# Kernel tuning notes

Hardware: AMD Instinct MI355X
Metric: run time of the kernel (lower is better)

Reference implementation:

```python
import jax, jax.numpy as jnp
import numpy as np

DIM = 1024
D_INNER = 2048

def setup_inputs() -> dict:
    key = jax.random.key(0)
    ks = jax.random.split(key, 8)
    B, T = 8, 1024
    x = jax.random.normal(ks[0], (B, T, DIM), dtype=jnp.float32)
    h0 = jnp.zeros((B, D_INNER), dtype=jnp.float32)
    # params (xavier-ish scales)
    in_proj_w = jax.random.normal(ks[1], (D_INNER, DIM), dtype=jnp.float32) * (2.0 / (DIM + D_INNER)) ** 0.5
    out_proj_w = jax.random.normal(ks[2], (DIM, D_INNER), dtype=jnp.float32) * (2.0 / (DIM + D_INNER)) ** 0.5
    c_h = jax.random.uniform(ks[3], (D_INNER,), jnp.float32, -0.1, 0.1)
    # spectral normalization as in _init_weights
    c_h = c_h * jnp.minimum(1.0, 0.99 / jnp.abs(jnp.fft.fft(c_h)).max())
    c_x = jax.random.uniform(ks[4], (D_INNER,), jnp.float32, -0.1, 0.1)
    c_x = c_x * jnp.minimum(1.0, 0.99 / jnp.abs(jnp.fft.fft(c_x)).max())
    b = jnp.zeros((D_INNER,), dtype=jnp.float32)
    W_gate = jax.random.normal(ks[5], (D_INNER, D_INNER), dtype=jnp.float32) * (1.0 / D_INNER) ** 0.5
    b_gate = jnp.zeros((D_INNER,), dtype=jnp.float32)
    return {"x": x, "h0": h0, "in_proj_w": in_proj_w, "out_proj_w": out_proj_w,
            "c_h": c_h, "c_x": c_x, "b": b, "W_gate": W_gate, "b_gate": b_gate}

def _circ_apply_fft(fft_c, v):
    # circ(c) @ v along last axis via real FFT; v: [..., D]
    D = v.shape[-1]
    return jnp.fft.irfft(fft_c * jnp.fft.rfft(v, axis=-1), n=D, axis=-1)

def reference(x, h0, in_proj_w, out_proj_w, c_h, c_x, b, W_gate, b_gate):
    B, T, _ = x.shape
    D = h0.shape[-1]
    x_proj = jnp.einsum('btd,ed->bte', x, in_proj_w)  # [B,T,D_inner]
    # gate path (fully parallel over T)
    gate = jax.nn.silu(jnp.einsum('bte,fe->btf', x_proj, W_gate) + b_gate)
    # input circulant contribution, parallel over all tokens
    pre = _circ_apply_fft(jnp.fft.rfft(c_x), x_proj) + b  # [B,T,D]
    fft_ch = jnp.fft.rfft(c_h)

    def step(h_prev, pre_t):
        h_new = jnp.tanh(_circ_apply_fft(fft_ch, h_prev) + pre_t)
        return h_new, h_new

    pre_tbd = jnp.transpose(pre, (1, 0, 2))  # [T,B,D]
    h_final, h_seq = jax.lax.scan(step, h0, pre_tbd)  # h_seq: [T,B,D]
    cell_out = jnp.transpose(h_seq, (1, 0, 2)) * gate  # [B,T,D]
    output = jnp.einsum('bte,de->btd', cell_out, out_proj_w)  # [B,T,dim]
    return output, h_final
```

## Files before the change

kernel.cpp:

```cpp
#include <hip/hip_runtime.h>
#include <cstdint>
#include <cstddef>

#define DI 2048
#define DM 1024
#define BB 8
#define TT 1024
#define ROWS (BB*TT)

typedef short  short8 __attribute__((ext_vector_type(8)));
typedef float  f32x4  __attribute__((ext_vector_type(4)));
typedef float  f32x16 __attribute__((ext_vector_type(16)));

__device__ __forceinline__ unsigned short f2bf(float f) {
  unsigned int u = __builtin_bit_cast(unsigned int, f);
  u = u + 0x7fffu + ((u >> 16) & 1u);
  return (unsigned short)(u >> 16);
}
__device__ __forceinline__ float fast_tanh(float x) {
  float ax = fabsf(x);
  float e  = __expf(-2.0f * ax);
  float t  = (1.0f - e) / (1.0f + e);
  return x < 0.0f ? -t : t;
}
__device__ __forceinline__ float silu_f(float z) {
  return z / (1.0f + __expf(-z));
}
__device__ __forceinline__ unsigned mulpk(unsigned a, unsigned b) {
  float a0 = __builtin_bit_cast(float, a << 16);
  float a1 = __builtin_bit_cast(float, a & 0xffff0000u);
  float b0 = __builtin_bit_cast(float, b << 16);
  float b1 = __builtin_bit_cast(float, b & 0xffff0000u);
  unsigned r0 = f2bf(a0 * b0), r1 = f2bf(a1 * b1);
  return r0 | (r1 << 16);
}
__device__ __forceinline__ uint4 pack8(const unsigned short* q) {
  uint4 p;
  p.x = (unsigned)q[0] | ((unsigned)q[1] << 16);
  p.y = (unsigned)q[2] | ((unsigned)q[3] << 16);
  p.z = (unsigned)q[4] | ((unsigned)q[5] << 16);
  p.w = (unsigned)q[6] | ((unsigned)q[7] << 16);
  return p;
}

__global__ void cast_k(const float* __restrict__ s, short* __restrict__ d, int n4) {
  int i = blockIdx.x * 256 + threadIdx.x;
  if (i >= n4) return;
  float4 f = ((const float4*)s)[i];
  unsigned lo = (unsigned)f2bf(f.x) | ((unsigned)f2bf(f.y) << 16);
  unsigned hi = (unsigned)f2bf(f.z) | ((unsigned)f2bf(f.w) << 16);
  uint2 o; o.x = lo; o.y = hi;
  ((uint2*)d)[i] = o;
}

__global__ void build_cx_k(const float* __restrict__ cx, short* __restrict__ C) {
  int tid = blockIdx.x * 256 + threadIdx.x;
  int n   = tid >> 8;
  int k0  = (tid & 255) * 8;
  unsigned short q[8];
#pragma unroll
  for (int j = 0; j < 8; ++j) q[j] = f2bf(cx[(n - (k0 + j)) & (DI - 1)]);
  *(uint4*)(C + (size_t)n * DI + k0) = pack8(q);
}

__global__ __launch_bounds__(256) void gemm_k(
    const short* __restrict__ A, const short* __restrict__ A2,
    const short* __restrict__ Bt,
    int M, int N, int K, int mode, const float* __restrict__ bias,
    float* __restrict__ outF, short* __restrict__ outH)
{
  __shared__ __align__(16) short As[128 * 40];
  __shared__ __align__(16) short Bs[128 * 40];
  const int tid  = threadIdx.x;
  const int m0   = blockIdx.y * 128, n0 = blockIdx.x * 128;
  const int wave = tid >> 6, lane = tid & 63;
  const int wy = wave >> 1, wx = wave & 1;
  const int l = lane & 15, G = lane >> 4;
  const int srow = tid >> 1, sseg = tid & 1;

  f32x4 acc[4][4];
#pragma unroll
  for (int i = 0; i < 4; ++i)
#pragma unroll
    for (int j = 0; j < 4; ++j) acc[i][j] = (f32x4){0.f, 0.f, 0.f, 0.f};

  for (int k0 = 0; k0 < K; k0 += 32) {
    if (k0) __syncthreads();
    const short* ga = A  + (size_t)(m0 + srow) * K + k0 + sseg * 16;
    const short* gb = Bt + (size_t)(n0 + srow) * K + k0 + sseg * 16;
    uint4 a0 = *(const uint4*)ga;
    uint4 a1 = *(const uint4*)(ga + 8);
    if (A2) {
      const short* g2 = A2 + (size_t)(m0 + srow) * K + k0 + sseg * 16;
      uint4 m0v = *(const uint4*)g2;
      uint4 m1v = *(const uint4*)(g2 + 8);
      a0.x = mulpk(a0.x, m0v.x); a0.y = mulpk(a0.y, m0v.y);
      a0.z = mulpk(a0.z, m0v.z); a0.w = mulpk(a0.w, m0v.w);
      a1.x = mulpk(a1.x, m1v.x); a1.y = mulpk(a1.y, m1v.y);
      a1.z = mulpk(a1.z, m1v.z); a1.w = mulpk(a1.w, m1v.w);
    }
    uint4 b0 = *(const uint4*)gb;
    uint4 b1 = *(const uint4*)(gb + 8);
    *(uint4*)&As[srow * 40 + sseg * 16]     = a0;
    *(uint4*)&As[srow * 40 + sseg * 16 + 8] = a1;
    *(uint4*)&Bs[srow * 40 + sseg * 16]     = b0;
    *(uint4*)&Bs[srow * 40 + sseg * 16 + 8] = b1;
    __syncthreads();
    short8 af[4], bfv[4];
#pragma unroll
    for (int i = 0; i < 4; ++i) af[i]  = *(const short8*)&As[(64 * wy + 16 * i + l) * 40 + 8 * G];
#pragma unroll
    for (int j = 0; j < 4; ++j) bfv[j] = *(const short8*)&Bs[(64 * wx + 16 * j + l) * 40 + 8 * G];
#pragma unroll
    for (int i = 0; i < 4; ++i)
#pragma unroll
      for (int j = 0; j < 4; ++j)
        acc[i][j] = __builtin_amdgcn_mfma_f32_16x16x32_bf16(af[i], bfv[j], acc[i][j], 0, 0, 0);
  }

#pragma unroll
  for (int j = 0; j < 4; ++j) {
    const int c = n0 + 64 * wx + 16 * j + l;
    float bv = 0.f;
    if (mode == 1 || mode == 2) bv = bias[c];
#pragma unroll
    for (int i = 0; i < 4; ++i) {
      const int r0 = m0 + 64 * wy + 16 * i + 4 * G;
#pragma unroll
      for (int v = 0; v < 4; ++v) {
        float z = acc[i][j][v] + bv;
        size_t off = (size_t)(r0 + v) * N + c;
        if (mode == 0)      outH[off] = (short)f2bf(z);
        else if (mode == 2) outH[off] = (short)f2bf(silu_f(z));
        else                outF[off] = z;
      }
    }
  }
}

__global__ __launch_bounds__(512, 2) void fused_k(
    const float* __restrict__ pre, const float* __restrict__ h0,
    const float* __restrict__ ch, short* __restrict__ hseq,
    float* __restrict__ hfin,
    const short* __restrict__ xproj, const short* __restrict__ wg,
    const float* __restrict__ bg, short* __restrict__ gate)
{
  __shared__ __align__(16) char smem[53248];
  const int bid = blockIdx.x;
  const int tid = threadIdx.x;

  if (bid < BB) {
    short* h_lds   = (short*)smem;
    float* pre_lds = (float*)(smem + 4096);
    float* part    = (float*)(smem + 20480);
    const int b = bid;
    const int wid = tid >> 6, lane = tid & 63;
    const int nh = wid & 1, kg = wid >> 1;
    const int L = lane & 31, G2 = lane >> 5;
    const int q = 32 * nh + L;
    const float* preB = pre + (size_t)b * TT * DI;

    short8 av[32];
#pragma unroll
    for (int i = 0; i < 32; ++i) {
      const int kbase = 16 * (32 * kg + i) + 8 * G2;
      short8 v;
#pragma unroll
      for (int j = 0; j < 8; ++j)
        v[j] = (short)f2bf(ch[(L - kbase - j) & (DI - 1)]);
      av[i] = v;
    }

    {
      const int n0 = 4 * tid;
      float4 hv = *(const float4*)(h0 + b * DI + n0);
      unsigned lo = (unsigned)f2bf(hv.x) | ((unsigned)f2bf(hv.y) << 16);
      unsigned hi = (unsigned)f2bf(hv.z) | ((unsigned)f2bf(hv.w) << 16);
      const int blk = tid >> 1;
      const int pblk = blk ^ ((blk >> 3) & 7);
      uint2 w; w.x = lo; w.y = hi;
      *(uint2*)&h_lds[pblk * 8 + 4 * (tid & 1)] = w;
      *(float4*)&pre_lds[n0] = *(const float4*)(preB + n0);
    }
    __syncthreads();

    const int cbase = (G2 + 4 * q + 64 * kg) & 255;

    for (int t = 0; t < TT; ++t) {
      const int cur = t & 1;
      const float* pn = preB + (size_t)(t + 1 < TT ? t + 1 : t) * DI;
      float4 pf = *(const float4*)(pn + 4 * tid);

      f32x16 acc0, acc1;
#pragma unroll
      for (int v = 0; v < 16; ++v) { acc0[v] = 0.f; acc1[v] = 0.f; }
#pragma unroll
      for (int i = 0; i < 32; i += 2) {
        int blkA = (cbase + 2 * i) & 255;
        int blkB = (cbase + 2 * i + 2) & 255;
        int pA = blkA ^ ((blkA >> 3) & 7);
        int pB = blkB ^ ((blkB >> 3) & 7);
        short8 bvA = *(const short8*)&h_lds[pA * 8];
        short8 bvB = *(const short8*)&h_lds[pB * 8];
        acc0 = __builtin_amdgcn_mfma_f32_32x32x16_bf16(av[i],     bvA, acc0, 0, 0, 0);
        acc1 = __builtin_amdgcn_mfma_f32_32x32x16_bf16(av[i + 1], bvB, acc1, 0, 0, 0);
      }
      {
        float* pk = part + kg * DI;
#pragma unroll
        for (int s = 0; s < 4; ++s) {
          const int blk4 = 2 * s + G2 + 8 * q;
          const int p4 = blk4 ^ ((blk4 >> 3) & 7);
          float4 w;
          w.x = acc0[4 * s + 0] + acc1[4 * s + 0];
          w.y = acc0[4 * s + 1] + acc1[4 * s + 1];
          w.z = acc0[4 * s + 2] + acc1[4 * s + 2];
          w.w = acc0[4 * s + 3] + acc1[4 * s + 3];
          *(float4*)&pk[4 * p4] = w;
        }
        *(float4*)&pre_lds[(cur ^ 1) * DI + 4 * tid] = pf;
      }
      __syncthreads();
      {
        const int pb = tid ^ ((tid >> 3) & 7);
        float4 c0 = *(const float4*)&part[4 * pb];
        float4 c1 = *(const float4*)&part[DI + 4 * pb];
        float4 c2 = *(const float4*)&part[2 * DI + 4 * pb];
        float4 c3 = *(const float4*)&part[3 * DI + 4 * pb];
        float4 pr = *(const float4*)&pre_lds[cur * DI + 4 * tid];
        float z0 = c0.x + c1.x + c2.x + c3.x + pr.x;
        float z1 = c0.y + c1.y + c2.y + c3.y + pr.y;
        float z2 = c0.z + c1.z + c2.z + c3.z + pr.z;
        float z3 = c0.w + c1.w + c2.w + c3.w + pr.w;
        float t0 = fast_tanh(z0), t1 = fast_tanh(z1);
        float t2 = fast_tanh(z2), t3 = fast_tanh(z3);
        unsigned lo = (unsigned)f2bf(t0) | ((unsigned)f2bf(t1) << 16);
        unsigned hi = (unsigned)f2bf(t2) | ((unsigned)f2bf(t3) << 16);
        const int blk = tid >> 1;
        const int pblk = blk ^ ((blk >> 3) & 7);
        uint2 w; w.x = lo; w.y = hi;
        *(uint2*)&h_lds[pblk * 8 + 4 * (tid & 1)] = w;
        *(uint2*)(hseq + (size_t)(b * TT + t) * DI + 4 * tid) = w;
        if (t == TT - 1) {
          float4 hf; hf.x = t0; hf.y = t1; hf.z = t2; hf.w = t3;
          *(float4*)(hfin + b * DI + 4 * tid) = hf;
        }
      }
      __syncthreads();
    }
  } else {
    short* As = (short*)smem;
    short* Bs = (short*)(smem + 20480);
    const int wid = tid >> 6, lane = tid & 63;
    const int wy = wid >> 1, wx = wid & 1;
    const int l = lane & 15, G = lane >> 4;

    for (int tile = bid - BB; tile < 512; tile += 248) {
      const int m0 = (tile & 31) * 256, n0 = (tile >> 5) * 128;
      f32x4 acc[4][4];
#pragma unroll
      for (int i = 0; i < 4; ++i)
#pragma unroll
        for (int j = 0; j < 4; ++j) acc[i][j] = (f32x4){0.f, 0.f, 0.f, 0.f};

      for (int k0 = 0; k0 < DI; k0 += 32) {
        __syncthreads();
        const short* ga = xproj + (size_t)(m0 + (tid >> 1)) * DI + k0 + (tid & 1) * 16;
        const short* gb = wg    + (size_t)(n0 + (tid >> 2)) * DI + k0 + (tid & 3) * 8;
        uint4 a0 = *(const uint4*)ga;
        uint4 a1 = *(const uint4*)(ga + 8);
        uint4 b0 = *(const uint4*)gb;
        *(uint4*)&As[(tid >> 1) * 40 + (tid & 1) * 16]     = a0;
        *(uint4*)&As[(tid >> 1) * 40 + (tid & 1) * 16 + 8] = a1;
        *(uint4*)&Bs[(tid >> 2) * 40 + (tid & 3) * 8]      = b0;
        __syncthreads();
        short8 af[4], bfv[4];
#pragma unroll
        for (int i = 0; i < 4; ++i) af[i]  = *(const short8*)&As[(64 * wy + 16 * i + l) * 40 + 8 * G];
#pragma unroll
        for (int j = 0; j < 4; ++j) bfv[j] = *(const short8*)&Bs[(64 * wx + 16 * j + l) * 40 + 8 * G];
#pragma unroll
        for (int i = 0; i < 4; ++i)
#pragma unroll
          for (int j = 0; j < 4; ++j)
            acc[i][j] = __builtin_amdgcn_mfma_f32_16x16x32_bf16(af[i], bfv[j], acc[i][j], 0, 0, 0);
      }
#pragma unroll
      for (int j = 0; j < 4; ++j) {
        const int c = n0 + 64 * wx + 16 * j + l;
        const float bv = bg[c];
#pragma unroll
        for (int i = 0; i < 4; ++i) {
          const int r0 = m0 + 64 * wy + 16 * i + 4 * G;
#pragma unroll
          for (int v = 0; v < 4; ++v) {
            float z = acc[i][j][v] + bv;
            gate[(size_t)(r0 + v) * DI + c] = (short)f2bf(silu_f(z));
          }
        }
      }
      __syncthreads();
    }
  }
}

extern "C" void kernel_launch(void* const* d_in, const int* in_sizes, int n_in,
                              void* d_out, int out_size, void* d_ws, size_t ws_size,
                              hipStream_t stream) {
  const float* x    = (const float*)d_in[0];
  const float* h0   = (const float*)d_in[1];
  const float* win  = (const float*)d_in[2];
  const float* wout = (const float*)d_in[3];
  const float* ch   = (const float*)d_in[4];
  const float* cx   = (const float*)d_in[5];
  const float* bb   = (const float*)d_in[6];
  const float* wg   = (const float*)d_in[7];
  const float* bg   = (const float*)d_in[8];
  float* out = (float*)d_out;

  char* ws = (char*)d_ws;
  short* o_xb    = (short*)(ws + 0);
  short* o_win   = (short*)(ws + 16777216);
  short* o_cx    = (short*)(ws + 20971520);
  short* o_hseq  = (short*)(ws + 0);
  short* o_xproj = (short*)(ws + 33554432);
  float* o_pre   = (float*)(ws + 67108864);
  short* o_wout  = (short*)(ws + 67108864);
  short* o_gate  = (short*)(ws + 134217728);
  short* o_wg    = (short*)(ws + 167772160);

  cast_k<<<8192, 256, 0, stream>>>(x,   o_xb,  (BB * TT * DM) / 4);
  cast_k<<<2048, 256, 0, stream>>>(win, o_win, (DI * DM) / 4);
  cast_k<<<4096, 256, 0, stream>>>(wg,  o_wg,  (DI * DI) / 4);
  build_cx_k<<<2048, 256, 0, stream>>>(cx, o_cx);

  gemm_k<<<dim3(DI / 128, ROWS / 128), 256, 0, stream>>>(
      o_xb, nullptr, o_win, ROWS, DI, DM, 0, nullptr, nullptr, o_xproj);

  gemm_k<<<dim3(DI / 128, ROWS / 128), 256, 0, stream>>>(
      o_xproj, nullptr, o_cx, ROWS, DI, DI, 1, bb, o_pre, nullptr);

  fused_k<<<256, 512, 0, stream>>>(o_pre, h0, ch, o_hseq,
                                   out + (size_t)BB * TT * DM,
                                   o_xproj, o_wg, bg, o_gate);

  cast_k<<<2048, 256, 0, stream>>>(wout, o_wout, (DM * DI) / 4);

  gemm_k<<<dim3(DM / 128, ROWS / 128), 256, 0, stream>>>(
      o_hseq, o_gate, o_wout, ROWS, DM, DI, 3, nullptr, out, nullptr);
}
```

Baseline: 2.140 ms.

## Rework recurrent circulant matvec to 16x16x32 MFMA with Toeplitz fragment reuse

The recurrent step's circulant matvec switches from 32x32x16 MFMAs over 32 precomputed A fragments to 16x16x32 MFMAs. The new form exploits the Toeplitz structure, so 22 register fragments are shared across 8 output tiles per k-step. Each of the 8 waves now owns a K-slice, which gives 8 partial-sum buffers reduced through a larger LDS region. The next-step pre values stay in a register instead of a double-buffered LDS array. This cuts per-step fragment registers and h loads, at the cost of a wider 8-way reduction and more LDS.

```diff
diff --git a/kernel.cpp b/kernel.cpp
--- a/kernel.cpp
+++ b/kernel.cpp
@@ -10,7 +10,6 @@
 
 typedef short  short8 __attribute__((ext_vector_type(8)));
 typedef float  f32x4  __attribute__((ext_vector_type(4)));
-typedef float  f32x16 __attribute__((ext_vector_type(16)));
 
 __device__ __forceinline__ unsigned short f2bf(float f) {
   unsigned int u = __builtin_bit_cast(unsigned int, f);
@@ -145,101 +144,97 @@
     const short* __restrict__ xproj, const short* __restrict__ wg,
     const float* __restrict__ bg, short* __restrict__ gate)
 {
-  __shared__ __align__(16) char smem[53248];
+  __shared__ __align__(16) char smem[69632];
   const int bid = blockIdx.x;
   const int tid = threadIdx.x;
 
   if (bid < BB) {
-    short* h_lds   = (short*)smem;
-    float* pre_lds = (float*)(smem + 4096);
-    float* part    = (float*)(smem + 20480);
-    const int b = bid;
-    const int wid = tid >> 6, lane = tid & 63;
-    const int nh = wid & 1, kg = wid >> 1;
-    const int L = lane & 31, G2 = lane >> 5;
-    const int q = 32 * nh + L;
+    short* h_lds = (short*)smem;
+    float* part  = (float*)(smem + 4096);
+    const int b    = bid;
+    const int kg   = tid >> 6;
+    const int lane = tid & 63;
+    const int q    = lane & 15;
+    const int G    = lane >> 4;
     const float* preB = pre + (size_t)b * TT * DI;
 
-    short8 av[32];
-#pragma unroll
-    for (int i = 0; i < 32; ++i) {
-      const int kbase = 16 * (32 * kg + i) + 8 * G2;
+    short8 av[22];
+#pragma unroll
+    for (int idx = 0; idx < 22; ++idx) {
+      const int base = 16 * (idx - 14) + q - 8 * G - 256 * kg;
       short8 v;
 #pragma unroll
       for (int j = 0; j < 8; ++j)
-        v[j] = (short)f2bf(ch[(L - kbase - j) & (DI - 1)]);
-      av[i] = v;
+        v[j] = (short)f2bf(ch[(base - j) & (DI - 1)]);
+      av[idx] = v;
     }
 
     {
-      const int n0 = 4 * tid;
-      float4 hv = *(const float4*)(h0 + b * DI + n0);
+      float4 hv = *(const float4*)(h0 + b * DI + 4 * tid);
       unsigned lo = (unsigned)f2bf(hv.x) | ((unsigned)f2bf(hv.y) << 16);
       unsigned hi = (unsigned)f2bf(hv.z) | ((unsigned)f2bf(hv.w) << 16);
       const int blk = tid >> 1;
-      const int pblk = blk ^ ((blk >> 3) & 7);
+      const int pb  = blk ^ ((blk >> 4) & 7);
       uint2 w; w.x = lo; w.y = hi;
-      *(uint2*)&h_lds[pblk * 8 + 4 * (tid & 1)] = w;
-      *(float4*)&pre_lds[n0] = *(const float4*)(preB + n0);
-    }
+      *(uint2*)&h_lds[pb * 8 + 4 * (tid & 1)] = w;
+    }
+    float4 pcur = *(const float4*)(preB + 4 * tid);
     __syncthreads();
 
-    const int cbase = (G2 + 4 * q + 64 * kg) & 255;
+    const int rbase = 32 * kg + G + 16 * q;
 
     for (int t = 0; t < TT; ++t) {
-      const int cur = t & 1;
       const float* pn = preB + (size_t)(t + 1 < TT ? t + 1 : t) * DI;
       float4 pf = *(const float4*)(pn + 4 * tid);
 
-      f32x16 acc0, acc1;
-#pragma unroll
-      for (int v = 0; v < 16; ++v) { acc0[v] = 0.f; acc1[v] = 0.f; }
-#pragma unroll
-      for (int i = 0; i < 32; i += 2) {
-        int blkA = (cbase + 2 * i) & 255;
-        int blkB = (cbase + 2 * i + 2) & 255;
-        int pA = blkA ^ ((blkA >> 3) & 7);
-        int pB = blkB ^ ((blkB >> 3) & 7);
-        short8 bvA = *(const short8*)&h_lds[pA * 8];
-        short8 bvB = *(const short8*)&h_lds[pB * 8];
-        acc0 = __builtin_amdgcn_mfma_f32_32x32x16_bf16(av[i],     bvA, acc0, 0, 0, 0);
-        acc1 = __builtin_amdgcn_mfma_f32_32x32x16_bf16(av[i + 1], bvB, acc1, 0, 0, 0);
-      }
+      f32x4 acc[8];
+#pragma unroll
+      for (int mt = 0; mt < 8; ++mt) acc[mt] = (f32x4){0.f, 0.f, 0.f, 0.f};
+
+#pragma unroll
+      for (int s = 0; s < 8; ++s) {
+        const int blk = (rbase + 4 * s) & 255;
+        const int pb  = blk ^ ((blk >> 4) & 7);
+        short8 bv = *(const short8*)&h_lds[pb * 8];
+#pragma unroll
+        for (int mt = 0; mt < 8; ++mt)
+          acc[mt] = __builtin_amdgcn_mfma_f32_16x16x32_bf16(av[mt - 2 * s + 14], bv, acc[mt], 0, 0, 0);
+      }
+
       {
-        float* pk = part + kg * DI;
-#pragma unroll
-        for (int s = 0; s < 4; ++s) {
-          const int blk4 = 2 * s + G2 + 8 * q;
-          const int p4 = blk4 ^ ((blk4 >> 3) & 7);
-          float4 w;
-          w.x = acc0[4 * s + 0] + acc1[4 * s + 0];
-          w.y = acc0[4 * s + 1] + acc1[4 * s + 1];
-          w.z = acc0[4 * s + 2] + acc1[4 * s + 2];
-          w.w = acc0[4 * s + 3] + acc1[4 * s + 3];
-          *(float4*)&pk[4 * p4] = w;
+        float* pk = part + (kg << 11);
+#pragma unroll
+        for (int mt = 0; mt < 8; ++mt) {
+          const int nb  = 4 * mt + G + 32 * q;
+          const int pnb = nb ^ ((nb >> 5) & 7);
+          *(f32x4*)&pk[4 * pnb] = acc[mt];
         }
-        *(float4*)&pre_lds[(cur ^ 1) * DI + 4 * tid] = pf;
       }
       __syncthreads();
+
       {
-        const int pb = tid ^ ((tid >> 3) & 7);
-        float4 c0 = *(const float4*)&part[4 * pb];
-        float4 c1 = *(const float4*)&part[DI + 4 * pb];
-        float4 c2 = *(const float4*)&part[2 * DI + 4 * pb];
-        float4 c3 = *(const float4*)&part[3 * DI + 4 * pb];
-        float4 pr = *(const float4*)&pre_lds[cur * DI + 4 * tid];
-        float z0 = c0.x + c1.x + c2.x + c3.x + pr.x;
-        float z1 = c0.y + c1.y + c2.y + c3.y + pr.y;
-        float z2 = c0.z + c1.z + c2.z + c3.z + pr.z;
-        float z3 = c0.w + c1.w + c2.w + c3.w + pr.w;
+        const int pnb = tid ^ ((tid >> 5) & 7);
+        const float* pp = part + 4 * pnb;
+        float4 c0 = *(const float4*)(pp);
+        float4 c1 = *(const float4*)(pp + 2048);
+        float4 c2 = *(const float4*)(pp + 4096);
+        float4 c3 = *(const float4*)(pp + 6144);
+        float4 c4 = *(const float4*)(pp + 8192);
+        float4 c5 = *(const float4*)(pp + 10240);
+        float4 c6 = *(const float4*)(pp + 12288);
+        float4 c7 = *(const float4*)(pp + 14336);
+        float z0 = ((c0.x + c1.x) + (c2.x + c3.x)) + ((c4.x + c5.x) + (c6.x + c7.x)) + pcur.x;
+        float z1 = ((c0.y + c1.y) + (c2.y + c3.y)) + ((c4.y + c5.y) + (c6.y + c7.y)) + pcur.y;
+        float z2 = ((c0.z + c1.z) + (c2.z + c3.z)) + ((c4.z + c5.z) + (c6.z + c7.z)) + pcur.z;
+        float z3 = ((c0.w + c1.w) + (c2.w + c3.w)) + ((c4.w + c5.w) + (c6.w + c7.w)) + pcur.w;
         float t0 = fast_tanh(z0), t1 = fast_tanh(z1);
         float t2 = fast_tanh(z2), t3 = fast_tanh(z3);
         unsigned lo = (unsigned)f2bf(t0) | ((unsigned)f2bf(t1) << 16);
         unsigned hi = (unsigned)f2bf(t2) | ((unsigned)f2bf(t3) << 16);
         const int blk = tid >> 1;
-        const int pblk = blk ^ ((blk >> 3) & 7);
+        const int pb  = blk ^ ((blk >> 4) & 7);
         uint2 w; w.x = lo; w.y = hi;
-        *(uint2*)&h_lds[pblk * 8 + 4 * (tid & 1)] = w;
+        *(uint2*)&h_lds[pb * 8 + 4 * (tid & 1)] = w;
         *(uint2*)(hseq + (size_t)(b * TT + t) * DI + 4 * tid) = w;
         if (t == TT - 1) {
           float4 hf; hf.x = t0; hf.y = t1; hf.z = t2; hf.w = t3;
@@ -247,6 +242,7 @@
         }
       }
       __syncthreads();
+      pcur = pf;
     }
   } else {
     short* As = (short*)smem;
```

Result: slower. 2.290 ms (+7.0%).
